# Kernel tuning notes

Measured on AMD Instinct MI355X. Metric: run time of the kernel, lower is better.

Reference implementation:

```python
import jax, jax.numpy as jnp
import numpy as np

B = 1024
NQ = 14
NL = 4


def _apply_single(psi_t, gate, q):
    # psi_t: (B, 2, ..., 2) with NQ qubit axes; gate: (2,2) or (B,2,2) complex64
    psi_m = jnp.moveaxis(psi_t, q + 1, -1)
    if gate.ndim == 3:
        new = jnp.einsum('b...i,bji->b...j', psi_m, gate)
    else:
        new = jnp.einsum('b...i,ji->b...j', psi_m, gate)
    return jnp.moveaxis(new, -1, q + 1)


def _apply_cnot(psi_t, c, t):
    # CNOT(control=c, target=t): flip target amplitudes on the control=1 slice
    ca, ta = c + 1, t + 1
    c0 = jax.lax.index_in_dim(psi_t, 0, ca, keepdims=False)
    c1 = jax.lax.index_in_dim(psi_t, 1, ca, keepdims=False)
    ta2 = ta - 1 if ta > ca else ta  # target axis shifts after control axis removal
    c1 = jnp.flip(c1, axis=ta2)  # X on target
    return jnp.stack([c0, c1], axis=ca)


def _forward(inputs, weights):
    Bn, nq = inputs.shape
    nl = weights.shape[0]
    dim = 2 ** nq
    # |0...0> initial state
    psi = jnp.zeros((Bn, dim), dtype=jnp.complex64).at[:, 0].set(1.0)
    psi = psi.reshape((Bn,) + (2,) * nq)
    # RY(theta) per-sample encoding gates: (B, nq, 2, 2)
    c = jnp.cos(inputs / 2).astype(jnp.complex64)
    s = jnp.sin(inputs / 2).astype(jnp.complex64)
    ry = jnp.stack([jnp.stack([c, -s], -1), jnp.stack([s, c], -1)], -2)
    # RX(theta) variational gates: (nl, nq, 2, 2)
    cw = jnp.cos(weights / 2).astype(jnp.complex64)
    sw = jnp.sin(weights / 2).astype(jnp.complex64)
    rx = jnp.stack([jnp.stack([cw, -1j * sw], -1), jnp.stack([-1j * sw, cw], -1)], -2)
    # Encoding layer
    for i in range(nq):
        psi = _apply_single(psi, ry[:, i], i)
    # Variational layers: CNOT chain then RX on every qubit
    for layer in range(nl):
        for i in range(nq - 1):
            psi = _apply_cnot(psi, i, i + 1)
        for i in range(nq):
            psi = _apply_single(psi, rx[layer, i], i)
    # Pauli-Z expectation per qubit
    probs = psi.real ** 2 + psi.imag ** 2  # (B, 2, ..., 2) float32
    exps = []
    for i in range(nq):
        p = jnp.moveaxis(probs, i + 1, 1).reshape(Bn, 2, -1).sum(-1)
        exps.append(p[:, 0] - p[:, 1])
    return jnp.stack(exps, axis=1).astype(jnp.float32)


def setup_inputs() -> dict:
    key = jax.random.key(0)
    k1, k2 = jax.random.split(key)
    inputs = jax.random.normal(k1, (B, NQ), dtype=jnp.float32)
    weights = 0.1 * jax.random.normal(k2, (NL, NQ), dtype=jnp.float32)
    return {"inputs": inputs, "weights": weights}


def reference(inputs, weights):
    return _forward(inputs, weights)
```

## Files before the change

kernel.cpp:

```cpp
#include <hip/hip_runtime.h>
#include <hip/hip_fp16.h>


typedef float v2f __attribute__((ext_vector_type(2)));

constexpr int NQ  = 14;
constexpr int DIM = 1 << NQ;
constexpr int NT  = 512;
constexpr int APT = DIM / NT;
constexpr int NL  = 4;

#define RXREG(QBIT, ANGLE)                                              \
    {                                                                   \
        float s_, c_;                                                   \
        __sincosf(0.5f * (ANGLE), &s_, &c_);                            \
        v2f sp; sp.x = s_; sp.y = -s_;                                  \
        _Pragma("unroll")                                               \
        for (int o = 0; o < APT; ++o) {                                 \
            if (o & (1 << (QBIT))) continue;                            \
            const int o1 = o | (1 << (QBIT));                           \
            v2f w0 = a[o1].yx, w1 = a[o].yx;                            \
            a[o]  = __builtin_elementwise_fma(sp, w0, c_ * a[o]);       \
            a[o1] = __builtin_elementwise_fma(sp, w1, c_ * a[o1]);      \
        }                                                               \
    }

#define SWEEP(WADDR, RADDR)                                             \
    {                                                                   \
        __half2* buf = lds + pb * DIM;                                  \
        _Pragma("unroll")                                               \
        for (int o = 0; o < APT; ++o)                                   \
            buf[WADDR] = __floats2half2_rn(a[o].x, a[o].y);             \
        __syncthreads();                                                \
        _Pragma("unroll")                                               \
        for (int o = 0; o < APT; ++o) {                                 \
            float2 f_ = __half22float2(buf[RADDR]);                     \
            a[o].x = f_.x; a[o].y = f_.y;                               \
        }                                                               \
        pb ^= 1;                                                        \
    }

__global__ __launch_bounds__(NT, 1)
void vqc_kernel(const float* __restrict__ inputs,
                const float* __restrict__ weights,
                float* __restrict__ out)
{
    extern __shared__ __half2 lds[];
    const int t    = threadIdx.x;
    const int b    = blockIdx.x;
    const int lane = t & 63;
    const int wv   = t >> 6;

    const int C_L0 = (t << 5) | ((t >> 1) & 31);
    const int Tp   = ((t << 5) ^ (t << 6)) & (DIM - 1);
    const int C_PR = Tp ^ ((Tp >> 6) & 31);
    const int C_L2 = (((t >> 5) << 10) | (t & 31)) ^ (((t >> 5) & 1) << 4);
    const int C_L1 = t ^ ((t >> 6) & 7);

    v2f a[APT];

    {
        float cs[NQ], sn[NQ];
#pragma unroll
        for (int q = 0; q < NQ; ++q)
            __sincosf(0.5f * inputs[b * NQ + q], &sn[q], &cs[q]);

        const int jbase = t << 5;
        const int srchi = (jbase ^ (jbase << 1)) & (DIM - 1);
        float base = 1.0f;
#pragma unroll
        for (int q = 6; q < NQ; ++q)
            base *= ((srchi >> q) & 1) ? sn[q] : cs[q];
#pragma unroll
        for (int o = 0; o < APT; ++o) {
            int j   = jbase | o;
            int src = (j ^ (j << 1)) & (DIM - 1);
            float v = base;
#pragma unroll
            for (int q = 0; q < 6; ++q)
                v *= ((src >> q) & 1) ? sn[q] : cs[q];
            a[o].x = v;
            a[o].y = 0.0f;
        }
    }

    int pb = 0;

#pragma unroll 1
    for (int layer = 0; layer < NL; ++layer) {
        const float* wl = weights + layer * NQ;

        if (layer > 0) {
            SWEEP(C_L1 ^ ((o << 9) | ((o & 3) << 3)), C_PR ^ (o ^ (o << 1)));
        }

#pragma unroll
        for (int q = 0; q < 5; ++q) RXREG(q, wl[q]);

        SWEEP(C_L0 ^ o, C_L2 ^ ((o << 5) | (o >> 1)));

#pragma unroll
        for (int q = 0; q < 5; ++q) RXREG(q, wl[5 + q]);

        SWEEP(C_L2 ^ ((o << 5) | (o >> 1)), C_L1 ^ ((o << 9) | ((o & 3) << 3)));

#pragma unroll
        for (int q = 10; q < NQ; ++q) RXREG(q - 9, wl[q]);
    }

    float ptot = 0.0f, Sq[5] = {0, 0, 0, 0, 0};
#pragma unroll
    for (int o = 0; o < APT; ++o) {
        float p = a[o].x * a[o].x + a[o].y * a[o].y;
        ptot += p;
#pragma unroll
        for (int m = 0; m < 5; ++m)
            Sq[m] += ((o >> m) & 1) ? -p : p;
    }

    float accL[6];
#pragma unroll
    for (int k = 0; k < 6; ++k) accL[k] = ptot;
#pragma unroll
    for (int k = 0; k < 6; ++k) {
        const int m = 1 << k;
#pragma unroll
        for (int j = 0; j < 6; ++j) {
            float pr = __shfl_xor(accL[j], m, 64);
            if (j == k)
                accL[j] = ((lane >> k) & 1) ? (pr - accL[j]) : (accL[j] - pr);
            else
                accL[j] += pr;
        }
        ptot += __shfl_xor(ptot, m, 64);
#pragma unroll
        for (int j = 0; j < 5; ++j) Sq[j] += __shfl_xor(Sq[j], m, 64);
    }

    float* red = reinterpret_cast<float*>(lds + DIM);
    if (lane == 0) {
        red[wv * 12 + 0] = ptot;
#pragma unroll
        for (int k = 0; k < 6; ++k) red[wv * 12 + 1 + k] = accL[k];
#pragma unroll
        for (int m = 0; m < 5; ++m) red[wv * 12 + 7 + m] = Sq[m];
    }
    __syncthreads();

    if (t < NQ) {
        float acc = 0.0f;
        if (t < 6) {
            for (int w = 0; w < 8; ++w) acc += red[w * 12 + 1 + t];
        } else if (t < 9) {
            const int bit = t - 6;
            for (int w = 0; w < 8; ++w) {
                float v = red[w * 12];
                acc += ((w >> bit) & 1) ? -v : v;
            }
        } else {
            for (int w = 0; w < 8; ++w) acc += red[w * 12 + 7 + (t - 9)];
        }
        out[b * NQ + t] = acc;
    }
}

extern "C" void kernel_launch(void* const* d_in, const int* in_sizes, int n_in,
                              void* d_out, int out_size, void* d_ws, size_t ws_size,
                              hipStream_t stream)
{
    const float* inputs  = (const float*)d_in[0];
    const float* weights = (const float*)d_in[1];
    float* out = (float*)d_out;

    const int Bn = in_sizes[0] / NQ;
    vqc_kernel<<<dim3(Bn), dim3(NT), 2 * DIM * sizeof(__half2), stream>>>(inputs, weights, out);
}
```

Baseline: 114.1 us.

## Process two samples per block, interleaving their LDS sweeps and RX gates

Each block now simulates two batch samples, ping-ponging between two LDS buffers so that one sample's RX gate arithmetic overlaps the other sample's LDS write/read transposes, with one barrier per half-step. The weight sin/cos values are precomputed once per block into a shared table instead of being recomputed by every thread. The grid is halved and per-thread register use doubles (two 32-amplitude state arrays), which risks spills and leaves fewer blocks to spread across CUs. The design assumes an even batch size.

Result: slower. 172.1 us (+50.9%).

```diff
diff --git a/kernel.cpp b/kernel.cpp
--- a/kernel.cpp
+++ b/kernel.cpp
@@ -10,34 +10,110 @@
 constexpr int APT = DIM / NT;
 constexpr int NL  = 4;
 
-#define RXREG(QBIT, ANGLE)                                              \
-    {                                                                   \
-        float s_, c_;                                                   \
-        __sincosf(0.5f * (ANGLE), &s_, &c_);                            \
-        v2f sp; sp.x = s_; sp.y = -s_;                                  \
+#define AD_PERMW (C_L1 ^ ((o << 9) | ((o & 3) << 3)))
+#define AD_PERMR (C_PR ^ (o ^ (o << 1)))
+#define AD_S1W   (C_L0 ^ o)
+#define AD_S1R   (C_L2 ^ ((o << 5) | (o >> 1)))
+#define AD_S2W   (C_L2 ^ ((o << 5) | (o >> 1)))
+#define AD_S2R   (C_L1 ^ ((o << 9) | ((o & 3) << 3)))
+
+#define WSWEEP(ARR, BUFI, WADDR)                                        \
+    {                                                                   \
+        __half2* buf_ = lds + (BUFI) * DIM;                             \
+        _Pragma("unroll")                                               \
+        for (int o = 0; o < APT; ++o)                                   \
+            buf_[WADDR] = __floats2half2_rn(ARR[o].x, ARR[o].y);        \
+    }
+
+#define RSWEEP(ARR, BUFI, RADDR)                                        \
+    {                                                                   \
+        __half2* buf_ = lds + (BUFI) * DIM;                             \
+        _Pragma("unroll")                                               \
+        for (int o = 0; o < APT; ++o) {                                 \
+            float2 f_ = __half22float2(buf_[RADDR]);                    \
+            ARR[o].x = f_.x; ARR[o].y = f_.y;                           \
+        }                                                               \
+    }
+
+#define RXQ(ARR, QBIT, SC)                                              \
+    {                                                                   \
+        v2f sp; sp.x = (SC).x; sp.y = -(SC).x;                          \
+        const float c_ = (SC).y;                                        \
         _Pragma("unroll")                                               \
         for (int o = 0; o < APT; ++o) {                                 \
             if (o & (1 << (QBIT))) continue;                            \
             const int o1 = o | (1 << (QBIT));                           \
-            v2f w0 = a[o1].yx, w1 = a[o].yx;                            \
-            a[o]  = __builtin_elementwise_fma(sp, w0, c_ * a[o]);       \
-            a[o1] = __builtin_elementwise_fma(sp, w1, c_ * a[o1]);      \
-        }                                                               \
-    }
-
-#define SWEEP(WADDR, RADDR)                                             \
-    {                                                                   \
-        __half2* buf = lds + pb * DIM;                                  \
-        _Pragma("unroll")                                               \
-        for (int o = 0; o < APT; ++o)                                   \
-            buf[WADDR] = __floats2half2_rn(a[o].x, a[o].y);             \
-        __syncthreads();                                                \
-        _Pragma("unroll")                                               \
-        for (int o = 0; o < APT; ++o) {                                 \
-            float2 f_ = __half22float2(buf[RADDR]);                     \
-            a[o].x = f_.x; a[o].y = f_.y;                               \
-        }                                                               \
-        pb ^= 1;                                                        \
+            v2f w0 = ARR[o1].yx, w1 = ARR[o].yx;                        \
+            ARR[o]  = __builtin_elementwise_fma(sp, w0, c_ * ARR[o]);   \
+            ARR[o1] = __builtin_elementwise_fma(sp, w1, c_ * ARR[o1]);  \
+        }                                                               \
+    }
+
+#define RX0_4(ARR, L)   { _Pragma("unroll") for (int q = 0; q < 5; ++q) { float2 sc_ = wtab[(L) * NQ + q];     RXQ(ARR, q,     sc_); } }
+#define RX5_9(ARR, L)   { _Pragma("unroll") for (int q = 0; q < 5; ++q) { float2 sc_ = wtab[(L) * NQ + 5 + q]; RXQ(ARR, q,     sc_); } }
+#define RX10_13(ARR, L) { _Pragma("unroll") for (int q = 10; q < NQ; ++q){ float2 sc_ = wtab[(L) * NQ + q];    RXQ(ARR, q - 9, sc_); } }
+
+#define ENCODE(ARR, ROWPTR)                                             \
+    {                                                                   \
+        float cs_[NQ], sn_[NQ];                                         \
+        _Pragma("unroll")                                               \
+        for (int q = 0; q < NQ; ++q)                                    \
+            __sincosf(0.5f * (ROWPTR)[q], &sn_[q], &cs_[q]);            \
+        const int jbase_ = t << 5;                                      \
+        const int srchi_ = (jbase_ ^ (jbase_ << 1)) & (DIM - 1);        \
+        float base_ = 1.0f;                                             \
+        _Pragma("unroll")                                               \
+        for (int q = 6; q < NQ; ++q)                                    \
+            base_ *= ((srchi_ >> q) & 1) ? sn_[q] : cs_[q];             \
+        _Pragma("unroll")                                               \
+        for (int o = 0; o < APT; ++o) {                                 \
+            int j_   = jbase_ | o;                                      \
+            int src_ = (j_ ^ (j_ << 1)) & (DIM - 1);                    \
+            float v_ = base_;                                           \
+            _Pragma("unroll")                                           \
+            for (int q = 0; q < 6; ++q)                                 \
+                v_ *= ((src_ >> q) & 1) ? sn_[q] : cs_[q];              \
+            ARR[o].x = v_; ARR[o].y = 0.0f;                             \
+        }                                                               \
+    }
+
+#define EXPECT(ARR, RED)                                                \
+    {                                                                   \
+        float ptot = 0.0f, Sq[5] = {0, 0, 0, 0, 0};                     \
+        _Pragma("unroll")                                               \
+        for (int o = 0; o < APT; ++o) {                                 \
+            float p = ARR[o].x * ARR[o].x + ARR[o].y * ARR[o].y;        \
+            ptot += p;                                                  \
+            _Pragma("unroll")                                           \
+            for (int m = 0; m < 5; ++m)                                 \
+                Sq[m] += ((o >> m) & 1) ? -p : p;                       \
+        }                                                               \
+        float accL[6];                                                  \
+        _Pragma("unroll")                                               \
+        for (int k = 0; k < 6; ++k) accL[k] = ptot;                     \
+        _Pragma("unroll")                                               \
+        for (int k = 0; k < 6; ++k) {                                   \
+            const int m_ = 1 << k;                                      \
+            _Pragma("unroll")                                           \
+            for (int j = 0; j < 6; ++j) {                               \
+                float pr = __shfl_xor(accL[j], m_, 64);                 \
+                if (j == k)                                             \
+                    accL[j] = ((lane >> k) & 1) ? (pr - accL[j])        \
+                                                : (accL[j] - pr);       \
+                else                                                    \
+                    accL[j] += pr;                                      \
+            }                                                           \
+            ptot += __shfl_xor(ptot, m_, 64);                           \
+            _Pragma("unroll")                                           \
+            for (int j = 0; j < 5; ++j) Sq[j] += __shfl_xor(Sq[j], m_, 64); \
+        }                                                               \
+        if (lane == 0) {                                                \
+            (RED)[wv * 12 + 0] = ptot;                                  \
+            _Pragma("unroll")                                           \
+            for (int k = 0; k < 6; ++k) (RED)[wv * 12 + 1 + k] = accL[k]; \
+            _Pragma("unroll")                                           \
+            for (int m = 0; m < 5; ++m) (RED)[wv * 12 + 7 + m] = Sq[m]; \
+        }                                                               \
     }
 
 __global__ __launch_bounds__(NT, 1)
@@ -50,6 +126,10 @@
     const int b    = blockIdx.x;
     const int lane = t & 63;
     const int wv   = t >> 6;
+    const int sA   = 2 * b, sB = 2 * b + 1;
+
+    float2* wtab = reinterpret_cast<float2*>(lds + 2 * DIM);
+    float*  red  = reinterpret_cast<float*>((char*)(lds + 2 * DIM) + 512);
 
     const int C_L0 = (t << 5) | ((t >> 1) & 31);
     const int Tp   = ((t << 5) ^ (t << 6)) & (DIM - 1);
@@ -57,110 +137,54 @@
     const int C_L2 = (((t >> 5) << 10) | (t & 31)) ^ (((t >> 5) & 1) << 4);
     const int C_L1 = t ^ ((t >> 6) & 7);
 
-    v2f a[APT];
-
-    {
-        float cs[NQ], sn[NQ];
-#pragma unroll
-        for (int q = 0; q < NQ; ++q)
-            __sincosf(0.5f * inputs[b * NQ + q], &sn[q], &cs[q]);
-
-        const int jbase = t << 5;
-        const int srchi = (jbase ^ (jbase << 1)) & (DIM - 1);
-        float base = 1.0f;
-#pragma unroll
-        for (int q = 6; q < NQ; ++q)
-            base *= ((srchi >> q) & 1) ? sn[q] : cs[q];
-#pragma unroll
-        for (int o = 0; o < APT; ++o) {
-            int j   = jbase | o;
-            int src = (j ^ (j << 1)) & (DIM - 1);
-            float v = base;
-#pragma unroll
-            for (int q = 0; q < 6; ++q)
-                v *= ((src >> q) & 1) ? sn[q] : cs[q];
-            a[o].x = v;
-            a[o].y = 0.0f;
-        }
-    }
-
-    int pb = 0;
+    if (t < NL * NQ) {
+        float s_, c_;
+        __sincosf(0.5f * weights[t], &s_, &c_);
+        wtab[t].x = s_; wtab[t].y = c_;
+    }
+
+    v2f aA[APT], aB[APT];
+    ENCODE(aA, inputs + sA * NQ);
+    ENCODE(aB, inputs + sB * NQ);
+    __syncthreads();
+
+    RX0_4(aA, 0);
+    WSWEEP(aA, 0, AD_S1W);  RX0_4(aB, 0);  __syncthreads();
+    RSWEEP(aA, 0, AD_S1R);  WSWEEP(aB, 1, AD_S1W);  RX5_9(aA, 0);  __syncthreads();
+    RSWEEP(aB, 1, AD_S1R);  WSWEEP(aA, 0, AD_S2W);  RX5_9(aB, 0);  __syncthreads();
+    RSWEEP(aA, 0, AD_S2R);  WSWEEP(aB, 1, AD_S2W);  RX10_13(aA, 0); __syncthreads();
 
 #pragma unroll 1
-    for (int layer = 0; layer < NL; ++layer) {
-        const float* wl = weights + layer * NQ;
-
-        if (layer > 0) {
-            SWEEP(C_L1 ^ ((o << 9) | ((o & 3) << 3)), C_PR ^ (o ^ (o << 1)));
-        }
-
-#pragma unroll
-        for (int q = 0; q < 5; ++q) RXREG(q, wl[q]);
-
-        SWEEP(C_L0 ^ o, C_L2 ^ ((o << 5) | (o >> 1)));
-
-#pragma unroll
-        for (int q = 0; q < 5; ++q) RXREG(q, wl[5 + q]);
-
-        SWEEP(C_L2 ^ ((o << 5) | (o >> 1)), C_L1 ^ ((o << 9) | ((o & 3) << 3)));
-
-#pragma unroll
-        for (int q = 10; q < NQ; ++q) RXREG(q - 9, wl[q]);
-    }
-
-    float ptot = 0.0f, Sq[5] = {0, 0, 0, 0, 0};
-#pragma unroll
-    for (int o = 0; o < APT; ++o) {
-        float p = a[o].x * a[o].x + a[o].y * a[o].y;
-        ptot += p;
-#pragma unroll
-        for (int m = 0; m < 5; ++m)
-            Sq[m] += ((o >> m) & 1) ? -p : p;
-    }
-
-    float accL[6];
-#pragma unroll
-    for (int k = 0; k < 6; ++k) accL[k] = ptot;
-#pragma unroll
-    for (int k = 0; k < 6; ++k) {
-        const int m = 1 << k;
-#pragma unroll
-        for (int j = 0; j < 6; ++j) {
-            float pr = __shfl_xor(accL[j], m, 64);
-            if (j == k)
-                accL[j] = ((lane >> k) & 1) ? (pr - accL[j]) : (accL[j] - pr);
-            else
-                accL[j] += pr;
-        }
-        ptot += __shfl_xor(ptot, m, 64);
-#pragma unroll
-        for (int j = 0; j < 5; ++j) Sq[j] += __shfl_xor(Sq[j], m, 64);
-    }
-
-    float* red = reinterpret_cast<float*>(lds + DIM);
-    if (lane == 0) {
-        red[wv * 12 + 0] = ptot;
-#pragma unroll
-        for (int k = 0; k < 6; ++k) red[wv * 12 + 1 + k] = accL[k];
-#pragma unroll
-        for (int m = 0; m < 5; ++m) red[wv * 12 + 7 + m] = Sq[m];
-    }
+    for (int l = 1; l < NL; ++l) {
+        RSWEEP(aB, 1, AD_S2R);  WSWEEP(aA, 0, AD_PERMW); RX10_13(aB, l - 1); __syncthreads();
+        RSWEEP(aA, 0, AD_PERMR); WSWEEP(aB, 1, AD_PERMW); RX0_4(aA, l);      __syncthreads();
+        RSWEEP(aB, 1, AD_PERMR); WSWEEP(aA, 0, AD_S1W);   RX0_4(aB, l);      __syncthreads();
+        RSWEEP(aA, 0, AD_S1R);   WSWEEP(aB, 1, AD_S1W);   RX5_9(aA, l);      __syncthreads();
+        RSWEEP(aB, 1, AD_S1R);   WSWEEP(aA, 0, AD_S2W);   RX5_9(aB, l);      __syncthreads();
+        RSWEEP(aA, 0, AD_S2R);   WSWEEP(aB, 1, AD_S2W);   RX10_13(aA, l);    __syncthreads();
+    }
+    RSWEEP(aB, 1, AD_S2R);  RX10_13(aB, NL - 1);
+
+    EXPECT(aA, red);
+    EXPECT(aB, red + 96);
     __syncthreads();
 
     if (t < NQ) {
-        float acc = 0.0f;
+        float accA = 0.0f, accB = 0.0f;
         if (t < 6) {
-            for (int w = 0; w < 8; ++w) acc += red[w * 12 + 1 + t];
+            for (int w = 0; w < 8; ++w) { accA += red[w * 12 + 1 + t]; accB += red[96 + w * 12 + 1 + t]; }
         } else if (t < 9) {
             const int bit = t - 6;
             for (int w = 0; w < 8; ++w) {
-                float v = red[w * 12];
-                acc += ((w >> bit) & 1) ? -v : v;
+                float vA = red[w * 12], vB = red[96 + w * 12];
+                accA += ((w >> bit) & 1) ? -vA : vA;
+                accB += ((w >> bit) & 1) ? -vB : vB;
             }
         } else {
-            for (int w = 0; w < 8; ++w) acc += red[w * 12 + 7 + (t - 9)];
+            for (int w = 0; w < 8; ++w) { accA += red[w * 12 + 7 + (t - 9)]; accB += red[96 + w * 12 + 7 + (t - 9)]; }
         }
-        out[b * NQ + t] = acc;
+        out[sA * NQ + t] = accA;
+        out[sB * NQ + t] = accB;
     }
 }
 
@@ -173,5 +197,6 @@
     float* out = (float*)d_out;
 
     const int Bn = in_sizes[0] / NQ;
-    vqc_kernel<<<dim3(Bn), dim3(NT), 2 * DIM * sizeof(__half2), stream>>>(inputs, weights, out);
+    const size_t shmem = 2 * DIM * sizeof(__half2) + 1536;
+    vqc_kernel<<<dim3(Bn / 2), dim3(NT), shmem, stream>>>(inputs, weights, out);
 }
```

## Redesign LDS transpose layouts with 64-bit accesses and precompute RX sin/cos table

Applied to the files above, without the earlier changes.

Replaces the three LDS sweep address schemes with new swizzled layouts so that reads (and some writes) move two half2 amplitudes at once as 64-bit uint2 accesses. The aim is fewer LDS instructions and fewer bank conflicts per sweep. RX gate sin/cos values are now computed once per block into a shared table instead of being recomputed by every thread for every gate, and the first layer is peeled out of the loop. The cost is more intricate index arithmetic, extra shared memory, and one extra barrier, and any error in the new permutations would give wrong results.

Result: faster. 109.4 us (-4.1%).

```diff
diff --git a/kernel.cpp b/kernel.cpp
--- a/kernel.cpp
+++ b/kernel.cpp
@@ -10,11 +10,20 @@
 constexpr int APT = DIM / NT;
 constexpr int NL  = 4;
 
-#define RXREG(QBIT, ANGLE)                                              \
-    {                                                                   \
-        float s_, c_;                                                   \
-        __sincosf(0.5f * (ANGLE), &s_, &c_);                            \
-        v2f sp; sp.x = s_; sp.y = -s_;                                  \
+static __device__ __forceinline__ unsigned pk(v2f v) {
+    __half2 h = __floats2half2_rn(v.x, v.y);
+    return *reinterpret_cast<unsigned*>(&h);
+}
+static __device__ __forceinline__ v2f upk(unsigned u) {
+    __half2 h = *reinterpret_cast<__half2*>(&u);
+    float2 f = __half22float2(h);
+    v2f r; r.x = f.x; r.y = f.y; return r;
+}
+
+#define RXQ(QBIT, SC)                                                   \
+    {                                                                   \
+        v2f sp; sp.x = (SC).x; sp.y = -(SC).x;                          \
+        const float c_ = (SC).y;                                        \
         _Pragma("unroll")                                               \
         for (int o = 0; o < APT; ++o) {                                 \
             if (o & (1 << (QBIT))) continue;                            \
@@ -25,16 +34,60 @@
         }                                                               \
     }
 
-#define SWEEP(WADDR, RADDR)                                             \
+#define RX0_4(L)   { _Pragma("unroll") for (int q = 0; q < 5; ++q)  { float2 sc_ = wtab[(L) * NQ + q];     RXQ(q, sc_); } }
+#define RX5_9(L)   { _Pragma("unroll") for (int q = 0; q < 5; ++q)  { float2 sc_ = wtab[(L) * NQ + 5 + q]; RXQ(q, sc_); } }
+#define RX10_13(L) { _Pragma("unroll") for (int q = 10; q < NQ; ++q){ float2 sc_ = wtab[(L) * NQ + q];     RXQ(q - 9, sc_); } }
+
+#define SWEEP_S1                                                        \
     {                                                                   \
         __half2* buf = lds + pb * DIM;                                  \
-        _Pragma("unroll")                                               \
-        for (int o = 0; o < APT; ++o)                                   \
-            buf[WADDR] = __floats2half2_rn(a[o].x, a[o].y);             \
+        uint2* buf64 = reinterpret_cast<uint2*>(buf);                   \
+        _Pragma("unroll")                                               \
+        for (int o = 0; o < APT; ++o) {                                 \
+            __half2 h = __floats2half2_rn(a[o].x, a[o].y);              \
+            buf[C1w ^ (((o & 15) << 1) | (o << 5))] = h;                \
+        }                                                               \
         __syncthreads();                                                \
         _Pragma("unroll")                                               \
+        for (int o = 0; o < APT; o += 2) {                              \
+            uint2 r_ = buf64[(C1r ^ o) >> 1];                           \
+            a[o] = upk(r_.x); a[o + 1] = upk(r_.y);                     \
+        }                                                               \
+        pb ^= 1;                                                        \
+    }
+
+#define SWEEP_S2                                                        \
+    {                                                                   \
+        uint2* buf64 = reinterpret_cast<uint2*>(lds + pb * DIM);        \
+        _Pragma("unroll")                                               \
+        for (int o = 0; o < 16; ++o)                                    \
+            buf64[(C2w ^ (o << 7)) >> 1] =                              \
+                make_uint2(pk(a[o]), pk(a[o + 16]));                    \
+        __syncthreads();                                                \
+        _Pragma("unroll")                                               \
+        for (int o = 0; o < APT; o += 2) {                              \
+            uint2 r_ = buf64[(C2r ^ ((((o >> 1) & 1) << 6)              \
+                                   | (((o >> 2) & 7) << 11))) >> 1];    \
+            a[o] = upk(r_.x); a[o + 1] = upk(r_.y);                     \
+        }                                                               \
+        pb ^= 1;                                                        \
+    }
+
+#define SWEEP_PERM                                                      \
+    {                                                                   \
+        __half2* buf = lds + pb * DIM;                                  \
+        uint2* buf64 = reinterpret_cast<uint2*>(buf);                   \
+        _Pragma("unroll")                                               \
+        for (int o = 0; o < APT; o += 2)                                \
+            buf64[(Cpw ^ (((o >> 1) & 15) << 10)) >> 1] =               \
+                make_uint2(pk(a[o]), pk(a[o + 1]));                     \
+        __syncthreads();                                                \
+        _Pragma("unroll")                                               \
         for (int o = 0; o < APT; ++o) {                                 \
-            float2 f_ = __half22float2(buf[RADDR]);                     \
+            const int O_   = (o ^ (o << 1)) & 0x3F;                     \
+            const int ApO_ = ((((O_ & 15) ^ ((O_ >> 5) & 15))) << 1)    \
+                           | ((O_ & 31) << 5);                          \
+            float2 f_ = __half22float2(buf[ApT ^ ApO_]);                \
             a[o].x = f_.x; a[o].y = f_.y;                               \
         }                                                               \
         pb ^= 1;                                                        \
@@ -51,11 +104,26 @@
     const int lane = t & 63;
     const int wv   = t >> 6;
 
-    const int C_L0 = (t << 5) | ((t >> 1) & 31);
-    const int Tp   = ((t << 5) ^ (t << 6)) & (DIM - 1);
-    const int C_PR = Tp ^ ((Tp >> 6) & 31);
-    const int C_L2 = (((t >> 5) << 10) | (t & 31)) ^ (((t >> 5) & 1) << 4);
-    const int C_L1 = t ^ ((t >> 6) & 7);
+    float2* wtab = reinterpret_cast<float2*>(lds + 2 * DIM);
+    float*  red  = reinterpret_cast<float*>((char*)(lds + 2 * DIM) + 512);
+
+    const int C1w = (t & 31) | (((t >> 5) & 15) << 10);
+    const int C1r = ((t & 15) << 1) | ((t & 31) << 5) | (((t >> 5) & 15) << 10);
+    const int C2w = ((t & 15) << 1) | (((t >> 4) & 1) << 5) | (((t >> 5) & 1) << 6)
+                  | (((t >> 6) & 7) << 11);
+    const int C2r = ((t & 15) << 1) | (((t >> 4) & 1) << 5) | (((t >> 5) & 15) << 7);
+    const int Cpw = (((t & 15) ^ ((t >> 5) & 15)) << 1) | ((t & 31) << 5);
+    const int Tm  = ((t << 5) ^ (t << 6)) & (DIM - 1);
+    const int ApT = ((Tm >> 9) & 1)
+                  | ((((Tm & 15) ^ ((Tm >> 5) & 15))) << 1)
+                  | ((Tm & 31) << 5)
+                  | (((Tm >> 10) & 15) << 10);
+
+    if (t < NL * NQ) {
+        float s_, c_;
+        __sincosf(0.5f * weights[t], &s_, &c_);
+        wtab[t].x = s_; wtab[t].y = c_;
+    }
 
     v2f a[APT];
 
@@ -79,33 +147,28 @@
 #pragma unroll
             for (int q = 0; q < 6; ++q)
                 v *= ((src >> q) & 1) ? sn[q] : cs[q];
-            a[o].x = v;
-            a[o].y = 0.0f;
+            a[o].x = v; a[o].y = 0.0f;
         }
     }
 
+    __syncthreads();
+
     int pb = 0;
 
+    RX0_4(0);
+    SWEEP_S1;
+    RX5_9(0);
+    SWEEP_S2;
+    RX10_13(0);
+
 #pragma unroll 1
-    for (int layer = 0; layer < NL; ++layer) {
-        const float* wl = weights + layer * NQ;
-
-        if (layer > 0) {
-            SWEEP(C_L1 ^ ((o << 9) | ((o & 3) << 3)), C_PR ^ (o ^ (o << 1)));
-        }
-
-#pragma unroll
-        for (int q = 0; q < 5; ++q) RXREG(q, wl[q]);
-
-        SWEEP(C_L0 ^ o, C_L2 ^ ((o << 5) | (o >> 1)));
-
-#pragma unroll
-        for (int q = 0; q < 5; ++q) RXREG(q, wl[5 + q]);
-
-        SWEEP(C_L2 ^ ((o << 5) | (o >> 1)), C_L1 ^ ((o << 9) | ((o & 3) << 3)));
-
-#pragma unroll
-        for (int q = 10; q < NQ; ++q) RXREG(q - 9, wl[q]);
+    for (int l = 1; l < NL; ++l) {
+        SWEEP_PERM;
+        RX0_4(l);
+        SWEEP_S1;
+        RX5_9(l);
+        SWEEP_S2;
+        RX10_13(l);
     }
 
     float ptot = 0.0f, Sq[5] = {0, 0, 0, 0, 0};
@@ -137,7 +200,6 @@
         for (int j = 0; j < 5; ++j) Sq[j] += __shfl_xor(Sq[j], m, 64);
     }
 
-    float* red = reinterpret_cast<float*>(lds + DIM);
     if (lane == 0) {
         red[wv * 12 + 0] = ptot;
 #pragma unroll
@@ -173,5 +235,6 @@
     float* out = (float*)d_out;
 
     const int Bn = in_sizes[0] / NQ;
-    vqc_kernel<<<dim3(Bn), dim3(NT), 2 * DIM * sizeof(__half2), stream>>>(inputs, weights, out);
-}
+    const size_t shmem = 2 * DIM * sizeof(__half2) + 1536;
+    vqc_kernel<<<dim3(Bn), dim3(NT), shmem, stream>>>(inputs, weights, out);
+}
```
